# Optimization experiments

Hardware: AMD Instinct MI355X
Metric: run time of the kernel (lower is better)

The kernel has to match this reference:

```python
import jax, jax.numpy as jnp
import numpy as np

H = 50  # hidden_size


def _lstm_layer(x_seq, W_ih, W_hh, b):
    """Single-layer LSTM over a full sequence.
    x_seq: [B, T, D]; W_ih: [4H, D]; W_hh: [4H, H]; b: [4H] (b_ih + b_hh).
    Gate order matches PyTorch: i, f, g, o. Returns hidden seq [B, T, H].
    """
    B = x_seq.shape[0]
    # Precompute the input projection for every timestep in one GEMM.
    xW = jnp.einsum('btd,gd->btg', x_seq, W_ih) + b          # [B, T, 4H]
    xW = jnp.swapaxes(xW, 0, 1)                              # [T, B, 4H] time-major for scan

    def step(carry, xg):
        h, c = carry
        gates = xg + h @ W_hh.T                              # [B, 4H]
        i, f, g, o = jnp.split(gates, 4, axis=-1)
        i = jax.nn.sigmoid(i)
        f = jax.nn.sigmoid(f)
        g = jnp.tanh(g)
        o = jax.nn.sigmoid(o)
        c = f * c + i * g
        h = o * jnp.tanh(c)
        return (h, c), h

    init = (jnp.zeros((B, H), x_seq.dtype), jnp.zeros((B, H), x_seq.dtype))
    _, hs = jax.lax.scan(step, init, xW)                     # hs: [T, B, H]
    return jnp.swapaxes(hs, 0, 1)                            # [B, T, H]


def setup_inputs() -> dict:
    key = jax.random.key(0)
    ks = jax.random.split(key, 9)
    B, T, D, O = 4096, 512, 2, 1
    s = 1.0 / np.sqrt(H)  # PyTorch LSTM init scale: U(-1/sqrt(H), 1/sqrt(H))
    u = lambda k, shape: jax.random.uniform(k, shape, jnp.float32, -s, s)
    return {
        'x': jax.random.normal(ks[0], (B, T, D), jnp.float32),
        'W_ih0': u(ks[1], (4 * H, D)),
        'W_hh0': u(ks[2], (4 * H, H)),
        'b0': u(ks[3], (4 * H,)),   # b_ih + b_hh folded into one bias (identical math)
        'W_ih1': u(ks[4], (4 * H, H)),
        'W_hh1': u(ks[5], (4 * H, H)),
        'b1': u(ks[6], (4 * H,)),
        'W_fc': u(ks[7], (O, H)),
        'b_fc': u(ks[8], (O,)),
    }


def reference(x, W_ih0, W_hh0, b0, W_ih1, W_hh1, b1, W_fc, b_fc):
    h0 = _lstm_layer(x, W_ih0, W_hh0, b0)    # [B, T, H] layer 0
    h1 = _lstm_layer(h0, W_ih1, W_hh1, b1)   # [B, T, H] layer 1
    # Final-step linear head: out = fc(out[:, -1, :])
    return h1[:, -1, :] @ W_fc.T + b_fc      # [B, 1]
```

## Files before the change

kernel.cpp:

```cpp
#include <hip/hip_runtime.h>


typedef _Float16 f16;
typedef f16  f16x8 __attribute__((ext_vector_type(8)));
typedef float f32x4 __attribute__((ext_vector_type(4)));
typedef unsigned short u16;
typedef unsigned int   u32;

#define TT   512
#define MB   16
#define KP   136
#define XTP  513
#define BLK  512

#define EXP2(v) __builtin_amdgcn_exp2f(v)
__device__ __forceinline__ float rcp_(float v) { return __builtin_amdgcn_rcpf(v); }

#define L2E  1.4426950408889634f
#define L2E2 2.8853900817779268f

__device__ __forceinline__ float welem(int layer, int g, int u, int k,
        const float* __restrict__ Wih0, const float* __restrict__ Whh0,
        const float* __restrict__ b0,
        const float* __restrict__ Wih1, const float* __restrict__ Whh1,
        const float* __restrict__ b1) {
    if (u >= 50) return 0.0f;
    const float s = (g == 2) ? L2E2 : -L2E;
    const int row = g * 50 + u;
    if (layer == 0) {
        if (k < 50)  return s * Whh0[row * 50 + k];
        if (k < 52)  return s * Wih0[row * 2 + (k - 50)];
        if (k == 52) return s * b0[row];
        return 0.0f;
    } else {
        if (k < 50)             return s * Wih1[row * 50 + k];
        if (k == 52)            return s * b1[row];
        if (k >= 64 && k < 114) return s * Whh1[row * 50 + (k - 64)];
        return 0.0f;
    }
}

#define EWFUSED(YI, YF, YG, YO, CS, HOUT)                                     \
    {                                                                         \
        const float eI = EXP2(YI);                                            \
        const float eF = EXP2(YF);                                            \
        const float eG = EXP2(YG);                                            \
        const float eO = EXP2(YO);                                            \
        const float fg  = rcp_(1.0f + eF);                                    \
        const float num = fmaf(L2E2, eG, -L2E2);                              \
        const float igg = num * rcp_((1.0f + eI) * (1.0f + eG));              \
        CS = fmaf(fg, CS, igg);                                               \
        const float cc = fminf(fmaxf(CS, -80.0f), 80.0f);                     \
        const float eC = EXP2(cc);                                            \
        HOUT = (eC - 1.0f) * rcp_((1.0f + eO) * (eC + 1.0f));                 \
    }

extern "C" __global__ void __launch_bounds__(BLK, 2)
lstm2_v9(const float* __restrict__ x,
         const float* __restrict__ W_ih0, const float* __restrict__ W_hh0,
         const float* __restrict__ b0,
         const float* __restrict__ W_ih1, const float* __restrict__ W_hh1,
         const float* __restrict__ b1,
         const float* __restrict__ W_fc,  const float* __restrict__ b_fc,
         float* __restrict__ out)
{
    __shared__ __align__(16) u16 hc[2][MB][KP];
    __shared__ u32   xpack[MB][XTP];
    __shared__ float hfin[MB][52];

    const int tid   = threadIdx.x;
    const int lane  = tid & 63;
    const int wid   = tid >> 6;
    const int layer = wid >> 2;
    const int ub    = wid & 3;
    const int col   = lane & 15;
    const int kg    = lane >> 4;
    const int bbase = blockIdx.x * MB;

    for (int idx = tid; idx < MB * TT; idx += BLK) {
        const int b = idx >> 9, t = idx & (TT - 1);
        const float2 v = *reinterpret_cast<const float2*>(
            x + ((size_t)(bbase + b) * TT + t) * 2);
        xpack[b][t] = (u32)__builtin_bit_cast(u16, (f16)v.x)
                    | ((u32)__builtin_bit_cast(u16, (f16)v.y) << 16);
    }
    {
        u32* hcU = reinterpret_cast<u32*>(&hc[0][0][0]);
        for (int i = tid; i < 2 * MB * KP / 2; i += BLK) hcU[i] = 0;
    }
    __syncthreads();
    if (tid < 32) hc[tid >> 4][tid & 15][52] = (u16)0x3C00;
    else if (tid < 48)
        *reinterpret_cast<u32*>(&hc[0][tid - 32][50]) = xpack[tid - 32][0];

    const int u = 16 * ub + col;
    f16x8 bf[4][4];
#pragma unroll
    for (int g = 0; g < 4; ++g) {
#pragma unroll
        for (int kf = 0; kf < 4; ++kf) {
            f16x8 v;
#pragma unroll
            for (int e = 0; e < 8; ++e)
                v[e] = (f16)welem(layer, g, u, kf * 32 + 8 * kg + e,
                                  W_ih0, W_hh0, b0, W_ih1, W_hh1, b1);
            bf[g][kf] = v;
        }
    }

    float cst[4] = {0.f, 0.f, 0.f, 0.f};
    const f32x4 z = {0.f, 0.f, 0.f, 0.f};
    __syncthreads();

    for (int it = 0; it <= TT; ++it) {
        const int p = it & 1, q = p ^ 1;
        f32x4 acc[4];

        if (layer == 0) {
            if (it < TT) {
                const f16x8 a0 = *reinterpret_cast<const f16x8*>(&hc[p][col][8 * kg]);
                const f16x8 a1 = *reinterpret_cast<const f16x8*>(&hc[p][col][32 + 8 * kg]);
                __builtin_amdgcn_s_setprio(1);
#pragma unroll
                for (int g = 0; g < 4; ++g) {
                    f32x4 c = __builtin_amdgcn_mfma_f32_16x16x32_f16(a0, bf[g][0], z, 0, 0, 0);
                    acc[g]  = __builtin_amdgcn_mfma_f32_16x16x32_f16(a1, bf[g][1], c, 0, 0, 0);
                }
                __builtin_amdgcn_s_setprio(0);
                if (u < 50) {
#pragma unroll
                    for (int r = 0; r < 4; ++r) {
                        float hv;
                        EWFUSED(acc[0][r], acc[1][r], acc[2][r], acc[3][r], cst[r], hv);
                        hc[q][4 * kg + r][u] = __builtin_bit_cast(u16, (f16)hv);
                    }
                }
            }
        } else {
            if (it >= 1) {
                const f16x8 a0 = *reinterpret_cast<const f16x8*>(&hc[p][col][8 * kg]);
                const f16x8 a1 = *reinterpret_cast<const f16x8*>(&hc[p][col][32 + 8 * kg]);
                const f16x8 a2 = *reinterpret_cast<const f16x8*>(&hc[p][col][64 + 8 * kg]);
                const f16x8 a3 = *reinterpret_cast<const f16x8*>(&hc[p][col][96 + 8 * kg]);
                __builtin_amdgcn_s_setprio(1);
#pragma unroll
                for (int g = 0; g < 4; ++g) {
                    f32x4 c = __builtin_amdgcn_mfma_f32_16x16x32_f16(a0, bf[g][0], z, 0, 0, 0);
                    c       = __builtin_amdgcn_mfma_f32_16x16x32_f16(a1, bf[g][1], c, 0, 0, 0);
                    c       = __builtin_amdgcn_mfma_f32_16x16x32_f16(a2, bf[g][2], c, 0, 0, 0);
                    acc[g]  = __builtin_amdgcn_mfma_f32_16x16x32_f16(a3, bf[g][3], c, 0, 0, 0);
                }
                __builtin_amdgcn_s_setprio(0);
                if (u < 50) {
#pragma unroll
                    for (int r = 0; r < 4; ++r) {
                        float hv;
                        EWFUSED(acc[0][r], acc[1][r], acc[2][r], acc[3][r], cst[r], hv);
                        hc[q][4 * kg + r][64 + u] = __builtin_bit_cast(u16, (f16)hv);
                        if (it == TT) hfin[4 * kg + r][u] = hv;
                    }
                }
            }
        }
        if (wid == 0 && lane < MB && (it + 1) < TT)
            *reinterpret_cast<u32*>(&hc[q][lane][50]) = xpack[lane][it + 1];

        __syncthreads();
    }

    if (tid < MB) {
        float d = b_fc[0];
#pragma unroll
        for (int uu = 0; uu < 50; ++uu) d = fmaf(W_fc[uu], hfin[tid][uu], d);
        out[bbase + tid] = d;
    }
}

extern "C" void kernel_launch(void* const* d_in, const int* in_sizes, int n_in,
                              void* d_out, int out_size, void* d_ws, size_t ws_size,
                              hipStream_t stream) {
    const float* x     = (const float*)d_in[0];
    const float* W_ih0 = (const float*)d_in[1];
    const float* W_hh0 = (const float*)d_in[2];
    const float* b0    = (const float*)d_in[3];
    const float* W_ih1 = (const float*)d_in[4];
    const float* W_hh1 = (const float*)d_in[5];
    const float* b1    = (const float*)d_in[6];
    const float* W_fc  = (const float*)d_in[7];
    const float* b_fc  = (const float*)d_in[8];
    float* out = (float*)d_out;

    const int B = in_sizes[0] / (TT * 2);
    dim3 grid(B / MB), block(BLK);
    hipLaunchKernelGGL(lstm2_v9, grid, block, 0, stream,
                       x, W_ih0, W_hh0, b0, W_ih1, W_hh1, b1, W_fc, b_fc, out);
}
```

Measured before the change: 373.4 us.

## Merge both LSTM layers into each wave with a 256-thread block

The block shrinks from 8 waves (4 per layer) to 4 waves, and each wave now computes both layer 0 and layer 1 for its 16-unit slice, holding both weight fragment sets in registers. The layer-1 MFMA chain is split into two independent accumulators that are summed afterwards, which shortens the dependency chain. The intent is to halve per-step barrier participants and interleave the two layers' MFMA and elementwise work within one wave for more latency hiding. In exchange, register pressure per wave rises and fewer waves are resident to hide latency.

```diff
diff --git a/kernel.cpp b/kernel.cpp
--- a/kernel.cpp
+++ b/kernel.cpp
@@ -11,7 +11,7 @@
 #define MB   16
 #define KP   136
 #define XTP  513
-#define BLK  512
+#define BLK  256
 
 #define EXP2(v) __builtin_amdgcn_exp2f(v)
 __device__ __forceinline__ float rcp_(float v) { return __builtin_amdgcn_rcpf(v); }
@@ -55,14 +55,14 @@
         HOUT = (eC - 1.0f) * rcp_((1.0f + eO) * (eC + 1.0f));                 \
     }
 
-extern "C" __global__ void __launch_bounds__(BLK, 2)
-lstm2_v9(const float* __restrict__ x,
-         const float* __restrict__ W_ih0, const float* __restrict__ W_hh0,
-         const float* __restrict__ b0,
-         const float* __restrict__ W_ih1, const float* __restrict__ W_hh1,
-         const float* __restrict__ b1,
-         const float* __restrict__ W_fc,  const float* __restrict__ b_fc,
-         float* __restrict__ out)
+extern "C" __global__ void __launch_bounds__(BLK, 1)
+lstm2_v10(const float* __restrict__ x,
+          const float* __restrict__ W_ih0, const float* __restrict__ W_hh0,
+          const float* __restrict__ b0,
+          const float* __restrict__ W_ih1, const float* __restrict__ W_hh1,
+          const float* __restrict__ b1,
+          const float* __restrict__ W_fc,  const float* __restrict__ b_fc,
+          float* __restrict__ out)
 {
     __shared__ __align__(16) u16 hc[2][MB][KP];
     __shared__ u32   xpack[MB][XTP];
@@ -71,8 +71,7 @@
     const int tid   = threadIdx.x;
     const int lane  = tid & 63;
     const int wid   = tid >> 6;
-    const int layer = wid >> 2;
-    const int ub    = wid & 3;
+    const int ub    = wid;
     const int col   = lane & 15;
     const int kg    = lane >> 4;
     const int bbase = blockIdx.x * MB;
@@ -94,71 +93,82 @@
         *reinterpret_cast<u32*>(&hc[0][tid - 32][50]) = xpack[tid - 32][0];
 
     const int u = 16 * ub + col;
-    f16x8 bf[4][4];
+    f16x8 bf0[4][2];
+    f16x8 bf1[4][4];
 #pragma unroll
     for (int g = 0; g < 4; ++g) {
+#pragma unroll
+        for (int kf = 0; kf < 2; ++kf) {
+            f16x8 v;
+#pragma unroll
+            for (int e = 0; e < 8; ++e)
+                v[e] = (f16)welem(0, g, u, kf * 32 + 8 * kg + e,
+                                  W_ih0, W_hh0, b0, W_ih1, W_hh1, b1);
+            bf0[g][kf] = v;
+        }
 #pragma unroll
         for (int kf = 0; kf < 4; ++kf) {
             f16x8 v;
 #pragma unroll
             for (int e = 0; e < 8; ++e)
-                v[e] = (f16)welem(layer, g, u, kf * 32 + 8 * kg + e,
+                v[e] = (f16)welem(1, g, u, kf * 32 + 8 * kg + e,
                                   W_ih0, W_hh0, b0, W_ih1, W_hh1, b1);
-            bf[g][kf] = v;
-        }
-    }
-
-    float cst[4] = {0.f, 0.f, 0.f, 0.f};
+            bf1[g][kf] = v;
+        }
+    }
+
+    float cst0[4] = {0.f, 0.f, 0.f, 0.f};
+    float cst1[4] = {0.f, 0.f, 0.f, 0.f};
     const f32x4 z = {0.f, 0.f, 0.f, 0.f};
     __syncthreads();
 
     for (int it = 0; it <= TT; ++it) {
         const int p = it & 1, q = p ^ 1;
-        f32x4 acc[4];
-
-        if (layer == 0) {
-            if (it < TT) {
-                const f16x8 a0 = *reinterpret_cast<const f16x8*>(&hc[p][col][8 * kg]);
-                const f16x8 a1 = *reinterpret_cast<const f16x8*>(&hc[p][col][32 + 8 * kg]);
-                __builtin_amdgcn_s_setprio(1);
-#pragma unroll
-                for (int g = 0; g < 4; ++g) {
-                    f32x4 c = __builtin_amdgcn_mfma_f32_16x16x32_f16(a0, bf[g][0], z, 0, 0, 0);
-                    acc[g]  = __builtin_amdgcn_mfma_f32_16x16x32_f16(a1, bf[g][1], c, 0, 0, 0);
+
+        const f16x8 a0 = *reinterpret_cast<const f16x8*>(&hc[p][col][8 * kg]);
+        const f16x8 a1 = *reinterpret_cast<const f16x8*>(&hc[p][col][32 + 8 * kg]);
+        const f16x8 a2 = *reinterpret_cast<const f16x8*>(&hc[p][col][64 + 8 * kg]);
+        const f16x8 a3 = *reinterpret_cast<const f16x8*>(&hc[p][col][96 + 8 * kg]);
+
+        f32x4 acc0[4], acc1[4];
+        const bool doL0 = (it < TT), doL1 = (it >= 1);
+
+        __builtin_amdgcn_s_setprio(1);
+        if (doL0) {
+#pragma unroll
+            for (int g = 0; g < 4; ++g) {
+                f32x4 c  = __builtin_amdgcn_mfma_f32_16x16x32_f16(a0, bf0[g][0], z, 0, 0, 0);
+                acc0[g]  = __builtin_amdgcn_mfma_f32_16x16x32_f16(a1, bf0[g][1], c, 0, 0, 0);
+            }
+        }
+        if (doL1) {
+#pragma unroll
+            for (int g = 0; g < 4; ++g) {
+                f32x4 cA = __builtin_amdgcn_mfma_f32_16x16x32_f16(a0, bf1[g][0], z, 0, 0, 0);
+                f32x4 cB = __builtin_amdgcn_mfma_f32_16x16x32_f16(a2, bf1[g][2], z, 0, 0, 0);
+                cA = __builtin_amdgcn_mfma_f32_16x16x32_f16(a1, bf1[g][1], cA, 0, 0, 0);
+                cB = __builtin_amdgcn_mfma_f32_16x16x32_f16(a3, bf1[g][3], cB, 0, 0, 0);
+                acc1[g] = cA + cB;
+            }
+        }
+        __builtin_amdgcn_s_setprio(0);
+
+        if (u < 50) {
+            if (doL0) {
+#pragma unroll
+                for (int r = 0; r < 4; ++r) {
+                    float hv;
+                    EWFUSED(acc0[0][r], acc0[1][r], acc0[2][r], acc0[3][r], cst0[r], hv);
+                    hc[q][4 * kg + r][u] = __builtin_bit_cast(u16, (f16)hv);
                 }
-                __builtin_amdgcn_s_setprio(0);
-                if (u < 50) {
-#pragma unroll
-                    for (int r = 0; r < 4; ++r) {
-                        float hv;
-                        EWFUSED(acc[0][r], acc[1][r], acc[2][r], acc[3][r], cst[r], hv);
-                        hc[q][4 * kg + r][u] = __builtin_bit_cast(u16, (f16)hv);
-                    }
-                }
-            }
-        } else {
-            if (it >= 1) {
-                const f16x8 a0 = *reinterpret_cast<const f16x8*>(&hc[p][col][8 * kg]);
-                const f16x8 a1 = *reinterpret_cast<const f16x8*>(&hc[p][col][32 + 8 * kg]);
-                const f16x8 a2 = *reinterpret_cast<const f16x8*>(&hc[p][col][64 + 8 * kg]);
-                const f16x8 a3 = *reinterpret_cast<const f16x8*>(&hc[p][col][96 + 8 * kg]);
-                __builtin_amdgcn_s_setprio(1);
-#pragma unroll
-                for (int g = 0; g < 4; ++g) {
-                    f32x4 c = __builtin_amdgcn_mfma_f32_16x16x32_f16(a0, bf[g][0], z, 0, 0, 0);
-                    c       = __builtin_amdgcn_mfma_f32_16x16x32_f16(a1, bf[g][1], c, 0, 0, 0);
-                    c       = __builtin_amdgcn_mfma_f32_16x16x32_f16(a2, bf[g][2], c, 0, 0, 0);
-                    acc[g]  = __builtin_amdgcn_mfma_f32_16x16x32_f16(a3, bf[g][3], c, 0, 0, 0);
-                }
-                __builtin_amdgcn_s_setprio(0);
-                if (u < 50) {
-#pragma unroll
-                    for (int r = 0; r < 4; ++r) {
-                        float hv;
-                        EWFUSED(acc[0][r], acc[1][r], acc[2][r], acc[3][r], cst[r], hv);
-                        hc[q][4 * kg + r][64 + u] = __builtin_bit_cast(u16, (f16)hv);
-                        if (it == TT) hfin[4 * kg + r][u] = hv;
-                    }
+            }
+            if (doL1) {
+#pragma unroll
+                for (int r = 0; r < 4; ++r) {
+                    float hv;
+                    EWFUSED(acc1[0][r], acc1[1][r], acc1[2][r], acc1[3][r], cst1[r], hv);
+                    hc[q][4 * kg + r][64 + u] = __builtin_bit_cast(u16, (f16)hv);
+                    if (it == TT) hfin[4 * kg + r][u] = hv;
                 }
             }
         }
@@ -192,6 +202,6 @@
 
     const int B = in_sizes[0] / (TT * 2);
     dim3 grid(B / MB), block(BLK);
-    hipLaunchKernelGGL(lstm2_v9, grid, block, 0, stream,
+    hipLaunchKernelGGL(lstm2_v10, grid, block, 0, stream,
                        x, W_ih0, W_hh0, b0, W_ih1, W_hh1, b1, W_fc, b_fc, out);
 }
```

Result: slower. 452.0 us (+21.0%).
